# Kernel optimization log

Hardware: AMD Instinct MI355X
Metric: run time of the kernel (lower is better)

Reference implementation:

```python
import jax, jax.numpy as jnp
import numpy as np

TEMPERATURE = 0.1
WEIGHT = 5.0
IS_SYMMETRIC = True


def setup_inputs() -> dict:
    key = jax.random.key(0)
    k1, k2, k3, k4, k5 = jax.random.split(key, 5)
    B, D = 2048, 128
    z_hat = jax.random.normal(k1, (1, B, D), dtype=jnp.float32)  # unused except batch size
    mu_x = jax.random.normal(k2, (B, D), dtype=jnp.float32)
    sigma_x = jax.random.uniform(k3, (B, D), minval=0.5, maxval=1.5, dtype=jnp.float32)
    mu_p = jax.random.normal(k4, (B, D), dtype=jnp.float32)
    sigma_p = jax.random.uniform(k5, (B, D), minval=0.5, maxval=1.5, dtype=jnp.float32)
    return {"z_hat": z_hat, "mu_x": mu_x, "sigma_x": sigma_x, "mu_p": mu_p, "sigma_p": sigma_p}


def _pairwise_kl(mus, sigmas):
    # K[a, b] = KL( N(mu_b, sig_b) || N(mu_a, sig_a) )  (matches torch repeat/repeat_interleave layout)
    D = mus.shape[1]
    var = sigmas * sigmas                      # [N, D]
    inv = 1.0 / var                            # [N, D]
    logdet = jnp.sum(jnp.log(sigmas), axis=1)  # [N]
    tr = jnp.einsum("ad,bd->ab", inv, var)                       # sum_d var_b / var_a
    quad = (jnp.einsum("ad,bd->ab", inv, mus * mus)
            - 2.0 * jnp.einsum("ad,bd->ab", mus * inv, mus)
            + jnp.sum(mus * mus * inv, axis=1)[:, None])         # sum_d (mu_b - mu_a)^2 / var_a
    return logdet[:, None] - logdet[None, :] + 0.5 * (tr + quad) - 0.5 * D


def reference(z_hat, mu_x, sigma_x, mu_p, sigma_p):
    B = mu_x.shape[0]
    N = 2 * B
    mus = jnp.concatenate([mu_x, mu_p], axis=0)       # [N, D]
    sigmas = jnp.concatenate([sigma_x, sigma_p], axis=0)

    logits = -_pairwise_kl(mus, sigmas)               # [N, N]
    if IS_SYMMETRIC:
        logits = (logits + logits.T) / 2
    logits = logits / TEMPERATURE

    # is_invariant=True: drop the diagonal -> [N, N-1] (static gather, jit-friendly)
    rows = jnp.arange(N)[:, None]
    cols = jnp.arange(N - 1)[None, :]
    idx = cols + (cols >= rows).astype(cols.dtype)    # skip column == row
    logits = jnp.take_along_axis(logits, jnp.broadcast_to(idx, (N, N - 1)), axis=1)

    n_classes = N - 1
    ar = jnp.arange(B)
    pos_idx = jnp.concatenate([ar + B - 1, ar], axis=0)  # [N]

    # weight != 1 branch: add -log(to_mult) at the positive logit of each row
    to_mult = (n_classes - 1.0 / WEIGHT) / (n_classes - 1)
    to_add = -jnp.log(jnp.asarray(to_mult, logits.dtype))
    logits = logits.at[jnp.arange(N), pos_idx].add(to_add)

    logp = jax.nn.log_softmax(logits, axis=1)
    hat_H_mlz = -jnp.mean(logp[jnp.arange(N), pos_idx])
    return hat_H_mlz
```

## Files before the change

### kernel.cpp

```cpp
#include <hip/hip_runtime.h>
#include <hip/hip_bf16.h>
#include <math.h>

typedef short bf16x8 __attribute__((ext_vector_type(8)));
typedef float f32x4 __attribute__((ext_vector_type(4)));

#define B_HALF 2048
#define N_TOT  4096
#define D_DIM  128
#define K_DIM  512
#define NGRP   32
#define NBLK   528
#define KSTEPS 16

__device__ unsigned red_done;

__global__ __launch_bounds__(256) void prep_feat(
    const float* __restrict__ mu_x, const float* __restrict__ sigma_x,
    const float* __restrict__ mu_p, const float* __restrict__ sigma_p,
    __hip_bfloat16* __restrict__ Gf, float* __restrict__ a) {
  const int tid = threadIdx.x;
  const int wv = tid >> 6;
  const int ln = tid & 63;
  const int d0 = ln * 2;
  const float SQ2 = 1.41421356237309515f;
#pragma unroll
  for (int rr = 0; rr < 16; rr += 4) {
    const int row = blockIdx.x * 16 + rr + wv;
    const float* mup = (row < B_HALF) ? mu_x : mu_p;
    const float* sgp = (row < B_HALF) ? sigma_x : sigma_p;
    const int gi = row & (B_HALF - 1);
    const float2 m2 = *(const float2*)(mup + gi * D_DIM + d0);
    const float2 s2 = *(const float2*)(sgp + gi * D_DIM + d0);
    float var0 = s2.x * s2.x, inv0 = 1.0f / var0, vm0 = var0 + m2.x * m2.x;
    float var1 = s2.y * s2.y, inv1 = 1.0f / var1, vm1 = var1 + m2.y * m2.y;
    size_t base = (size_t)row * K_DIM;
    __hip_bfloat162 h;
    unsigned ub;
#define PK2(OFF, X, Y)                                                        \
    h.x = __float2bfloat16(X); h.y = __float2bfloat16(Y);                     \
    __builtin_memcpy(&ub, &h, 4);                                             \
    __builtin_nontemporal_store(ub, (unsigned*)(Gf + base + (OFF) + d0));
    PK2(0,   inv0, inv1)
    PK2(128, vm0, vm1)
    PK2(256, SQ2 * m2.x * inv0, SQ2 * m2.y * inv1)
    PK2(384, -SQ2 * m2.x, -SQ2 * m2.y)
#undef PK2
    float av = m2.x * m2.x * inv0 + m2.y * m2.y * inv1;
#pragma unroll
    for (int x = 1; x < 64; x <<= 1) av += __shfl_xor(av, x);
    if (ln == 0) __builtin_nontemporal_store(av, &a[row]);
  }
}

#define GLOAD16(src, dst)                                                     \
  __builtin_amdgcn_global_load_lds(                                           \
      (const __attribute__((address_space(1))) void*)(src),                   \
      (__attribute__((address_space(3))) void*)(dst), 16, 0, 0)

__global__ __launch_bounds__(256, 3) void gemm_lse(
    const __hip_bfloat16* __restrict__ Gf, const float* __restrict__ a,
    float* __restrict__ lsep, float* __restrict__ pos, float to_add) {
  __shared__ char lt[3][128 * 64];
  __shared__ char rt[3][128 * 64];
  __shared__ float2 red[128][2];

  const int sb = (blockIdx.x & 7) * (NBLK / 8) + (blockIdx.x >> 3);
  int t = sb, rb = 0;
  while (t >= 32 - rb) { t -= 32 - rb; ++rb; }
  const int len = 32 - rb;
  const int cb = rb + ((rb & 1) ? (len - 1 - t) : t);

  const int tid  = threadIdx.x;
  const int lane = tid & 63;
  const int wave = tid >> 6;
  const int rowBase = rb * 128, colBase = cb * 128;
  const int wr = wave >> 1, wc = wave & 1;
  const int lx = lane & 15;
  const int rq = lane >> 4;

  f32x4 acc[4][4];
#pragma unroll
  for (int m = 0; m < 4; ++m)
#pragma unroll
    for (int n = 0; n < 4; ++n) acc[m][n] = (f32x4){0.f, 0.f, 0.f, 0.f};

  const int sr  = lane >> 2;
  const int scb = (((lane & 3) ^ (sr & 3)) << 4);
  const char* lsrc0 = (const char*)Gf + (size_t)rowBase * (K_DIM * 2);
  const char* rsrc0 = (const char*)Gf + (size_t)colBase * (K_DIM * 2);

#define STAGE(KK)                                                             \
  {                                                                           \
    const int b_ = (KK) % 3;                                                  \
    const char* ls_ = lsrc0 + (KK) * 64;                                      \
    const char* rs_ = rsrc0 + ((KK) ^ 4) * 64;                                \
    _Pragma("unroll")                                                         \
    for (int g = 0; g < 2; ++g) {                                             \
      const int row_ = wave * 32 + g * 16;                                    \
      GLOAD16(ls_ + (size_t)(row_ + sr) * 1024 + scb, &lt[b_][row_ * 64]);    \
      GLOAD16(rs_ + (size_t)(row_ + sr) * 1024 + scb, &rt[b_][row_ * 64]);    \
    }                                                                         \
  }

  STAGE(0)
  STAGE(1)

#pragma unroll
  for (int kk = 0; kk < KSTEPS; ++kk) {
    if (kk < KSTEPS - 1) asm volatile("s_waitcnt vmcnt(4)" ::: "memory");
    else                 asm volatile("s_waitcnt vmcnt(0)" ::: "memory");
    __builtin_amdgcn_s_barrier();
    __builtin_amdgcn_sched_barrier(0);
    if (kk + 2 < KSTEPS) STAGE(kk + 2)
    const int b = kk % 3;
    bf16x8 af[4], bg[4];
    const int kbp = ((rq ^ (lx & 3)) << 4);
#pragma unroll
    for (int m = 0; m < 4; ++m) {
      const int row = wr * 64 + m * 16 + lx;
      af[m] = *(const bf16x8*)(&lt[b][row * 64 + kbp]);
    }
#pragma unroll
    for (int n = 0; n < 4; ++n) {
      const int row = wc * 64 + n * 16 + lx;
      bg[n] = *(const bf16x8*)(&rt[b][row * 64 + kbp]);
    }
#pragma unroll
    for (int m = 0; m < 4; ++m)
#pragma unroll
      for (int n = 0; n < 4; ++n)
        acc[m][n] = __builtin_amdgcn_mfma_f32_16x16x32_bf16(af[m], bg[n], acc[m][n], 0, 0, 0);
  }
#undef STAGE

  const float c0 = 640.0f;
  const float c1 = 2.5f;
  float aR[4][4];
#pragma unroll
  for (int m = 0; m < 4; ++m)
#pragma unroll
    for (int v = 0; v < 4; ++v)
      aR[m][v] = a[rowBase + wr * 64 + m * 16 + rq * 4 + v];
  float aC[4];
#pragma unroll
  for (int n = 0; n < 4; ++n) aC[n] = a[colBase + wc * 64 + n * 16 + lx];

#pragma unroll
  for (int m = 0; m < 4; ++m)
#pragma unroll
    for (int n = 0; n < 4; ++n)
#pragma unroll
      for (int v = 0; v < 4; ++v) {
        int grow = rowBase + wr * 64 + m * 16 + rq * 4 + v;
        int gcol = colBase + wc * 64 + n * 16 + lx;
        float S = c0 - c1 * (acc[m][n][v] + aR[m][v] + aC[n]);
        if (gcol == grow) {
          S = -INFINITY;
        } else if (gcol == (grow ^ B_HALF)) {
          S += to_add;
          __builtin_nontemporal_store(S, &pos[grow]);
          __builtin_nontemporal_store(S, &pos[gcol]);
        }
        acc[m][n][v] = S;
      }

#pragma unroll
  for (int m = 0; m < 4; ++m)
#pragma unroll
    for (int v = 0; v < 4; ++v) {
      float pm = -INFINITY;
#pragma unroll
      for (int n = 0; n < 4; ++n) pm = fmaxf(pm, acc[m][n][v]);
#pragma unroll
      for (int x = 1; x < 16; x <<= 1) pm = fmaxf(pm, __shfl_xor(pm, x));
      float ps = 0.f;
#pragma unroll
      for (int n = 0; n < 4; ++n) ps += __expf(acc[m][n][v] - pm);
#pragma unroll
      for (int x = 1; x < 16; x <<= 1) ps += __shfl_xor(ps, x);
      if (lx == 0) red[wr * 64 + m * 16 + rq * 4 + v][wc] = make_float2(pm, ps);
    }
  __syncthreads();
  if (tid < 128) {
    float2 p0 = red[tid][0], p1 = red[tid][1];
    float M = fmaxf(p0.x, p1.x);
    float S = p0.y * __expf(p0.x - M) + p1.y * __expf(p1.x - M);
    __builtin_nontemporal_store(M + logf(S),
                                &lsep[(size_t)(rowBase + tid) * NGRP + cb]);
  }

  if (rb != cb) {
    __syncthreads();
#pragma unroll
    for (int n = 0; n < 4; ++n) {
      float cm = -INFINITY;
#pragma unroll
      for (int m = 0; m < 4; ++m)
#pragma unroll
        for (int v = 0; v < 4; ++v) cm = fmaxf(cm, acc[m][n][v]);
      cm = fmaxf(cm, __shfl_xor(cm, 16));
      cm = fmaxf(cm, __shfl_xor(cm, 32));
      float cs = 0.f;
#pragma unroll
      for (int m = 0; m < 4; ++m)
#pragma unroll
        for (int v = 0; v < 4; ++v) cs += __expf(acc[m][n][v] - cm);
      cs += __shfl_xor(cs, 16);
      cs += __shfl_xor(cs, 32);
      if (lane < 16) red[wc * 64 + n * 16 + lane][wr] = make_float2(cm, cs);
    }
    __syncthreads();
    if (tid < 128) {
      float2 p0 = red[tid][0], p1 = red[tid][1];
      float M = fmaxf(p0.x, p1.x);
      float S = p0.y * __expf(p0.x - M) + p1.y * __expf(p1.x - M);
      __builtin_nontemporal_store(M + logf(S),
                                  &lsep[(size_t)(colBase + tid) * NGRP + rb]);
    }
  }
}

__global__ __launch_bounds__(256) void reduce_final(
    const float* __restrict__ lsep, const float* __restrict__ pos,
    float* __restrict__ partial, float* __restrict__ out) {
  const int tid = threadIdx.x;
  const int row = blockIdx.x * 256 + tid;
  const float* lp = lsep + (size_t)row * NGRP;
  float M = lp[0];
#pragma unroll
  for (int k = 1; k < NGRP; ++k) M = fmaxf(M, lp[k]);
  float s = 0.f;
#pragma unroll
  for (int k = 0; k < NGRP; ++k) s += __expf(lp[k] - M);
  float contrib = (M + logf(s)) - pos[row];

  __shared__ float fr[256];
  fr[tid] = contrib;
  __syncthreads();
#pragma unroll
  for (int off = 128; off > 0; off >>= 1) {
    if (tid < off) fr[tid] += fr[tid + off];
    __syncthreads();
  }
  if (tid == 0) {
    partial[blockIdx.x] = fr[0];
    unsigned v = __hip_atomic_fetch_add(&red_done, 1u, __ATOMIC_ACQ_REL,
                                        __HIP_MEMORY_SCOPE_AGENT);
    if (v == 15u) {
      float tot = 0.f;
      for (int k = 0; k < 16; ++k) tot += partial[k];
      out[0] = tot * (1.0f / 4096.0f);
      __hip_atomic_store(&red_done, 0u, __ATOMIC_RELAXED,
                         __HIP_MEMORY_SCOPE_AGENT);
    }
  }
}

extern "C" void kernel_launch(void* const* d_in, const int* in_sizes, int n_in,
                              void* d_out, int out_size, void* d_ws, size_t ws_size,
                              hipStream_t stream) {
  const float* mu_x    = (const float*)d_in[1];
  const float* sigma_x = (const float*)d_in[2];
  const float* mu_p    = (const float*)d_in[3];
  const float* sigma_p = (const float*)d_in[4];
  float* out = (float*)d_out;

  float to_add = (float)(-log((4095.0 - 1.0 / 5.0) / 4094.0));

  const size_t featB = (size_t)N_TOT * K_DIM * 2;
  char* ws = (char*)d_ws;
  __hip_bfloat16* Gf = (__hip_bfloat16*)(ws);
  float* a       = (float*)(ws + featB);
  float* lsep    = (float*)(ws + featB + 16384);
  float* pos     = (float*)(ws + featB + 16384 + 524288);
  float* partial = (float*)(ws + featB + 16384 + 524288 + 16384);

  prep_feat<<<dim3(256), dim3(256), 0, stream>>>(mu_x, sigma_x, mu_p, sigma_p,
                                                 Gf, a);
  gemm_lse<<<dim3(NBLK), dim3(256), 0, stream>>>(Gf, a, lsep, pos, to_add);
  reduce_final<<<dim3(16), dim3(256), 0, stream>>>(lsep, pos, partial, out);
}
```

Baseline: 41.21 us.

## Fuse bf16 feature construction into GEMM tiles, dropping the feature buffer

The GEMM kernel now loads the fp32 mu and sigma tiles directly and builds the four bf16 feature blocks (inverse variance, var+mu², scaled mu/var, -scaled mu) in shared memory for each 32-wide d-chunk. The prep kernel only computes the per-row quadratic term. This removes the 4 MB intermediate write and re-read and shortens the prep kernel. In exchange every tile recomputes the features with reciprocals, uses plain register loads plus syncthreads double phases instead of the async global-to-LDS pipeline, and drops occupancy to 2 blocks per CU.

Result: slower. 50.25 us (+21.9%).

```diff
diff --git a/kernel.cpp b/kernel.cpp
--- a/kernel.cpp
+++ b/kernel.cpp
@@ -8,22 +8,19 @@
 #define B_HALF 2048
 #define N_TOT  4096
 #define D_DIM  128
-#define K_DIM  512
 #define NGRP   32
 #define NBLK   528
-#define KSTEPS 16
 
 __device__ unsigned red_done;
 
-__global__ __launch_bounds__(256) void prep_feat(
+__global__ __launch_bounds__(256) void prep_a(
     const float* __restrict__ mu_x, const float* __restrict__ sigma_x,
     const float* __restrict__ mu_p, const float* __restrict__ sigma_p,
-    __hip_bfloat16* __restrict__ Gf, float* __restrict__ a) {
+    float* __restrict__ a) {
   const int tid = threadIdx.x;
   const int wv = tid >> 6;
   const int ln = tid & 63;
   const int d0 = ln * 2;
-  const float SQ2 = 1.41421356237309515f;
 #pragma unroll
   for (int rr = 0; rr < 16; rr += 4) {
     const int row = blockIdx.x * 16 + rr + wv;
@@ -32,37 +29,24 @@
     const int gi = row & (B_HALF - 1);
     const float2 m2 = *(const float2*)(mup + gi * D_DIM + d0);
     const float2 s2 = *(const float2*)(sgp + gi * D_DIM + d0);
-    float var0 = s2.x * s2.x, inv0 = 1.0f / var0, vm0 = var0 + m2.x * m2.x;
-    float var1 = s2.y * s2.y, inv1 = 1.0f / var1, vm1 = var1 + m2.y * m2.y;
-    size_t base = (size_t)row * K_DIM;
-    __hip_bfloat162 h;
-    unsigned ub;
-#define PK2(OFF, X, Y)                                                        \
-    h.x = __float2bfloat16(X); h.y = __float2bfloat16(Y);                     \
-    __builtin_memcpy(&ub, &h, 4);                                             \
-    __builtin_nontemporal_store(ub, (unsigned*)(Gf + base + (OFF) + d0));
-    PK2(0,   inv0, inv1)
-    PK2(128, vm0, vm1)
-    PK2(256, SQ2 * m2.x * inv0, SQ2 * m2.y * inv1)
-    PK2(384, -SQ2 * m2.x, -SQ2 * m2.y)
-#undef PK2
-    float av = m2.x * m2.x * inv0 + m2.y * m2.y * inv1;
+    float av = m2.x * m2.x / (s2.x * s2.x) + m2.y * m2.y / (s2.y * s2.y);
 #pragma unroll
     for (int x = 1; x < 64; x <<= 1) av += __shfl_xor(av, x);
-    if (ln == 0) __builtin_nontemporal_store(av, &a[row]);
-  }
-}
-
-#define GLOAD16(src, dst)                                                     \
-  __builtin_amdgcn_global_load_lds(                                           \
-      (const __attribute__((address_space(1))) void*)(src),                   \
-      (__attribute__((address_space(3))) void*)(dst), 16, 0, 0)
-
-__global__ __launch_bounds__(256, 3) void gemm_lse(
-    const __hip_bfloat16* __restrict__ Gf, const float* __restrict__ a,
+    if (ln == 0) a[row] = av;
+  }
+}
+
+__device__ __forceinline__ short bfof(float v) {
+  __hip_bfloat16 h = __float2bfloat16(v);
+  return __builtin_bit_cast(short, h);
+}
+
+__global__ __launch_bounds__(256, 2) void gemm_lse(
+    const float* __restrict__ mu_x, const float* __restrict__ sigma_x,
+    const float* __restrict__ mu_p, const float* __restrict__ sigma_p,
+    const float* __restrict__ a,
     float* __restrict__ lsep, float* __restrict__ pos, float to_add) {
-  __shared__ char lt[3][128 * 64];
-  __shared__ char rt[3][128 * 64];
+  __shared__ short feat[2][4][128][32];
   __shared__ float2 red[128][2];
 
   const int sb = (blockIdx.x & 7) * (NBLK / 8) + (blockIdx.x >> 3);
@@ -78,6 +62,30 @@
   const int wr = wave >> 1, wc = wave & 1;
   const int lx = lane & 15;
   const int rq = lane >> 4;
+  const float SQ2 = 1.41421356237309515f;
+
+  const float* muR = (rowBase < B_HALF) ? mu_x + (size_t)rowBase * D_DIM
+                                        : mu_p + (size_t)(rowBase - B_HALF) * D_DIM;
+  const float* sgR = (rowBase < B_HALF) ? sigma_x + (size_t)rowBase * D_DIM
+                                        : sigma_p + (size_t)(rowBase - B_HALF) * D_DIM;
+  const float* muC = (colBase < B_HALF) ? mu_x + (size_t)colBase * D_DIM
+                                        : mu_p + (size_t)(colBase - B_HALF) * D_DIM;
+  const float* sgC = (colBase < B_HALF) ? sigma_x + (size_t)colBase * D_DIM
+                                        : sigma_p + (size_t)(colBase - B_HALF) * D_DIM;
+
+  int   sidev[4], rowv[4], pcv[4];
+  const float* mrow[4];
+  const float* srow[4];
+#pragma unroll
+  for (int it = 0; it < 4; ++it) {
+    const int idx = tid + it * 256;
+    const int side = idx >> 9, row = (idx >> 2) & 127, dg = idx & 3;
+    sidev[it] = side;
+    rowv[it]  = row;
+    pcv[it]   = dg ^ ((row >> 1) & 3);
+    mrow[it]  = (side ? muC : muR) + row * D_DIM + dg * 8;
+    srow[it]  = (side ? sgC : sgR) + row * D_DIM + dg * 8;
+  }
 
   f32x4 acc[4][4];
 #pragma unroll
@@ -85,54 +93,70 @@
 #pragma unroll
     for (int n = 0; n < 4; ++n) acc[m][n] = (f32x4){0.f, 0.f, 0.f, 0.f};
 
-  const int sr  = lane >> 2;
-  const int scb = (((lane & 3) ^ (sr & 3)) << 4);
-  const char* lsrc0 = (const char*)Gf + (size_t)rowBase * (K_DIM * 2);
-  const char* rsrc0 = (const char*)Gf + (size_t)colBase * (K_DIM * 2);
-
-#define STAGE(KK)                                                             \
-  {                                                                           \
-    const int b_ = (KK) % 3;                                                  \
-    const char* ls_ = lsrc0 + (KK) * 64;                                      \
-    const char* rs_ = rsrc0 + ((KK) ^ 4) * 64;                                \
+  float4 rm0[4], rm1[4], rs0[4], rs1[4];
+
+#define LOADC(DC)                                                             \
+  _Pragma("unroll")                                                           \
+  for (int it = 0; it < 4; ++it) {                                            \
+    rm0[it] = *(const float4*)(mrow[it] + (DC) * 32);                         \
+    rm1[it] = *(const float4*)(mrow[it] + (DC) * 32 + 4);                     \
+    rs0[it] = *(const float4*)(srow[it] + (DC) * 32);                         \
+    rs1[it] = *(const float4*)(srow[it] + (DC) * 32 + 4);                     \
+  }
+
+#define WRITEC()                                                              \
+  _Pragma("unroll")                                                           \
+  for (int it = 0; it < 4; ++it) {                                            \
+    float mv[8] = {rm0[it].x, rm0[it].y, rm0[it].z, rm0[it].w,                \
+                   rm1[it].x, rm1[it].y, rm1[it].z, rm1[it].w};               \
+    float sv[8] = {rs0[it].x, rs0[it].y, rs0[it].z, rs0[it].w,                \
+                   rs1[it].x, rs1[it].y, rs1[it].z, rs1[it].w};               \
+    bf16x8 o0, o1, o2, o3;                                                    \
     _Pragma("unroll")                                                         \
-    for (int g = 0; g < 2; ++g) {                                             \
-      const int row_ = wave * 32 + g * 16;                                    \
-      GLOAD16(ls_ + (size_t)(row_ + sr) * 1024 + scb, &lt[b_][row_ * 64]);    \
-      GLOAD16(rs_ + (size_t)(row_ + sr) * 1024 + scb, &rt[b_][row_ * 64]);    \
+    for (int j = 0; j < 8; ++j) {                                             \
+      float mu = mv[j], s = sv[j], var = s * s, inv;                          \
+      asm("v_rcp_f32 %0, %1" : "=v"(inv) : "v"(var));                         \
+      o0[j] = bfof(inv);                                                      \
+      o1[j] = bfof(var + mu * mu);                                            \
+      o2[j] = bfof(SQ2 * mu * inv);                                           \
+      o3[j] = bfof(-SQ2 * mu);                                                \
     }                                                                         \
-  }
-
-  STAGE(0)
-  STAGE(1)
-
-#pragma unroll
-  for (int kk = 0; kk < KSTEPS; ++kk) {
-    if (kk < KSTEPS - 1) asm volatile("s_waitcnt vmcnt(4)" ::: "memory");
-    else                 asm volatile("s_waitcnt vmcnt(0)" ::: "memory");
-    __builtin_amdgcn_s_barrier();
-    __builtin_amdgcn_sched_barrier(0);
-    if (kk + 2 < KSTEPS) STAGE(kk + 2)
-    const int b = kk % 3;
-    bf16x8 af[4], bg[4];
-    const int kbp = ((rq ^ (lx & 3)) << 4);
-#pragma unroll
-    for (int m = 0; m < 4; ++m) {
-      const int row = wr * 64 + m * 16 + lx;
-      af[m] = *(const bf16x8*)(&lt[b][row * 64 + kbp]);
-    }
-#pragma unroll
-    for (int n = 0; n < 4; ++n) {
-      const int row = wc * 64 + n * 16 + lx;
-      bg[n] = *(const bf16x8*)(&rt[b][row * 64 + kbp]);
-    }
-#pragma unroll
-    for (int m = 0; m < 4; ++m)
-#pragma unroll
-      for (int n = 0; n < 4; ++n)
-        acc[m][n] = __builtin_amdgcn_mfma_f32_16x16x32_bf16(af[m], bg[n], acc[m][n], 0, 0, 0);
-  }
-#undef STAGE
+    const int sd = sidev[it], rw = rowv[it], pc8 = pcv[it] * 8;               \
+    *(bf16x8*)&feat[sd][0 ^ sd][rw][pc8] = o0;                                \
+    *(bf16x8*)&feat[sd][1 ^ sd][rw][pc8] = o1;                                \
+    *(bf16x8*)&feat[sd][2 ^ sd][rw][pc8] = o2;                                \
+    *(bf16x8*)&feat[sd][3 ^ sd][rw][pc8] = o3;                                \
+  }
+
+  LOADC(0)
+#pragma unroll
+  for (int dc = 0; dc < 4; ++dc) {
+    __syncthreads();
+    WRITEC()
+    __syncthreads();
+    if (dc < 3) LOADC(dc + 1)
+#pragma unroll
+    for (int f = 0; f < 4; ++f) {
+      bf16x8 af[4], bg[4];
+#pragma unroll
+      for (int m = 0; m < 4; ++m) {
+        const int row = wr * 64 + m * 16 + lx;
+        af[m] = *(const bf16x8*)&feat[0][f][row][(rq ^ ((row >> 1) & 3)) * 8];
+      }
+#pragma unroll
+      for (int n = 0; n < 4; ++n) {
+        const int row = wc * 64 + n * 16 + lx;
+        bg[n] = *(const bf16x8*)&feat[1][f][row][(rq ^ ((row >> 1) & 3)) * 8];
+      }
+#pragma unroll
+      for (int m = 0; m < 4; ++m)
+#pragma unroll
+        for (int n = 0; n < 4; ++n)
+          acc[m][n] = __builtin_amdgcn_mfma_f32_16x16x32_bf16(af[m], bg[n], acc[m][n], 0, 0, 0);
+    }
+  }
+#undef LOADC
+#undef WRITEC
 
   const float c0 = 640.0f;
   const float c1 = 2.5f;
@@ -268,16 +292,14 @@
 
   float to_add = (float)(-log((4095.0 - 1.0 / 5.0) / 4094.0));
 
-  const size_t featB = (size_t)N_TOT * K_DIM * 2;
   char* ws = (char*)d_ws;
-  __hip_bfloat16* Gf = (__hip_bfloat16*)(ws);
-  float* a       = (float*)(ws + featB);
-  float* lsep    = (float*)(ws + featB + 16384);
-  float* pos     = (float*)(ws + featB + 16384 + 524288);
-  float* partial = (float*)(ws + featB + 16384 + 524288 + 16384);
-
-  prep_feat<<<dim3(256), dim3(256), 0, stream>>>(mu_x, sigma_x, mu_p, sigma_p,
-                                                 Gf, a);
-  gemm_lse<<<dim3(NBLK), dim3(256), 0, stream>>>(Gf, a, lsep, pos, to_add);
+  float* a       = (float*)(ws);
+  float* lsep    = (float*)(ws + 16384);
+  float* pos     = (float*)(ws + 16384 + 524288);
+  float* partial = (float*)(ws + 16384 + 524288 + 16384);
+
+  prep_a<<<dim3(256), dim3(256), 0, stream>>>(mu_x, sigma_x, mu_p, sigma_p, a);
+  gemm_lse<<<dim3(NBLK), dim3(256), 0, stream>>>(mu_x, sigma_x, mu_p, sigma_p,
+                                                 a, lsep, pos, to_add);
   reduce_final<<<dim3(16), dim3(256), 0, stream>>>(lsep, pos, partial, out);
 }
```
